# Optimization experiments

Measured on AMD Instinct MI355X. Metric: run time of the kernel, lower is better.

## Reference

```python
import jax, jax.numpy as jnp
import numpy as np

D_K = 128


def setup_inputs() -> dict:
    key = jax.random.key(0)
    k1, k2, k3, k4 = jax.random.split(key, 4)
    return {
        "value_in": jax.random.normal(k1, (4, 2048, 1024), dtype=jnp.float32),
        "w_q": jax.random.normal(k2, (1024, D_K), dtype=jnp.float32),
        "w_k": jax.random.normal(k3, (1024, D_K), dtype=jnp.float32),
        "w_v": jax.random.normal(k4, (1024, 128), dtype=jnp.float32),
    }


def reference(value_in, w_q, w_k, w_v):
    # Projections: [B,S,d_model] @ [d_model,d] -> [B,S,d]
    q = jnp.einsum('bsm,mk->bsk', value_in, w_q)
    k = jnp.einsum('bsm,mk->bsk', value_in, w_k)
    v = jnp.einsum('bsm,mv->bsv', value_in, w_v)
    # Scores [B,S,S], scaled by sqrt(d_k)
    scores = jnp.einsum('bqk,bsk->bqs', q, k) / jnp.sqrt(jnp.float32(D_K))
    S = scores.shape[-1]
    # Causal mask: keep lower triangle (q_idx >= k_idx), -inf elsewhere
    causal = jnp.tril(jnp.ones((S, S), dtype=bool))
    scores = jnp.where(causal, scores, -jnp.inf)
    # NOTE: softmax over the QUERY axis (dim=-2), not the key axis
    attention = jax.nn.softmax(scores, axis=-2)
    out = jnp.einsum('bqs,bsv->bqv', attention, v)
    return out, attention
```

## Files before the change

### kernel.cpp

```cpp
#include <hip/hip_runtime.h>
#include <math.h>

constexpr int B  = 4;
constexpr int S  = 2048;
constexpr int DM = 1024;
constexpr int DK = 128;
constexpr int BS = B * S;
constexpr int NSP = 8;
constexpr int QT  = 16;

static constexpr float SCALE = 0.08838834764831845f;

typedef __attribute__((ext_vector_type(8))) short bf16x8;
typedef __attribute__((ext_vector_type(4))) float f32x4;
typedef __attribute__((ext_vector_type(8))) unsigned short u16x8;

__device__ __forceinline__ unsigned short f2bf(float x) {
  unsigned u = __float_as_uint(x);
  unsigned r = (u + 0x7FFFu + ((u >> 16) & 1u)) >> 16;
  return (unsigned short)r;
}
__device__ __forceinline__ float bf2f(unsigned short h) {
  return __uint_as_float(((unsigned)h) << 16);
}

__device__ __forceinline__ void gload16(const void* g, void* l) {
  __builtin_amdgcn_global_load_lds(
      (const __attribute__((address_space(1))) void*)g,
      (__attribute__((address_space(3))) void*)l, 16, 0, 0);
}

__global__ __launch_bounds__(256) void cvt_hilo(
    const float* __restrict__ x, unsigned short* __restrict__ hi,
    unsigned short* __restrict__ lo)
{
  const size_t idx = (size_t)blockIdx.x * 256 + threadIdx.x;
  const float4 v = ((const float4*)x)[idx];
  ushort4 h, l;
  h.x = f2bf(v.x); l.x = f2bf(v.x - bf2f(h.x));
  h.y = f2bf(v.y); l.y = f2bf(v.y - bf2f(h.y));
  h.z = f2bf(v.z); l.z = f2bf(v.z - bf2f(h.z));
  h.w = f2bf(v.w); l.w = f2bf(v.w - bf2f(h.w));
  ((ushort4*)hi)[idx] = h;
  ((ushort4*)lo)[idx] = l;
}

__global__ void cvtw_kernel(const float* __restrict__ wq, const float* __restrict__ wk,
                            const float* __restrict__ wv,
                            unsigned short* __restrict__ Wth, unsigned short* __restrict__ Wtl)
{
  const int n = blockIdx.x;
  const int p = n >> 7, c = n & 127;
  const float* w = (p == 0) ? wq : (p == 1) ? wk : wv;
  for (int k = threadIdx.x; k < DM; k += 256) {
    const float x = w[(size_t)k * DK + c];
    const unsigned short h = f2bf(x);
    Wth[(size_t)n * DM + k] = h;
    Wtl[(size_t)n * DM + k] = f2bf(x - bf2f(h));
  }
}

__global__ __launch_bounds__(256) void proj_mfma(
    const unsigned short* __restrict__ Ah, const unsigned short* __restrict__ Al,
    const unsigned short* __restrict__ Wh, const unsigned short* __restrict__ Wl,
    unsigned short* __restrict__ qh, unsigned short* __restrict__ ql,
    unsigned short* __restrict__ kh, unsigned short* __restrict__ kl,
    float* __restrict__ vtmp)
{
  __shared__ unsigned short Ash[2][64 * 64];
  __shared__ unsigned short Wsh[2][64 * 64];

  const int r0 = blockIdx.x * 64;
  const int n0 = blockIdx.y * 64;
  const int t  = threadIdx.x;
  const int l  = t & 63, w = t >> 6;
  const int wm = w >> 1, wn = w & 1;
  const int fr = l & 15, kg = l >> 4;

  f32x4 acc[2][2] = {};

  for (int k0 = 0; k0 < DM; k0 += 64) {
    #pragma unroll
    for (int i = 0; i < 2; ++i) {
      const int flat = t + i * 256;
      const int row = flat >> 3, sg = flat & 7;
      const int sgs = sg ^ (row & 7);
      const size_t ga = (size_t)(r0 + row) * DM + k0 + sgs * 8;
      const size_t gw = (size_t)(n0 + row) * DM + k0 + sgs * 8;
      gload16(Ah + ga, &Ash[0][flat * 8]);
      gload16(Al + ga, &Ash[1][flat * 8]);
      gload16(Wh + gw, &Wsh[0][flat * 8]);
      gload16(Wl + gw, &Wsh[1][flat * 8]);
    }
    __syncthreads();

    #pragma unroll
    for (int kk = 0; kk < 2; ++kk) {
      bf16x8 ah[2], al[2], bh[2], bl[2];
      #pragma unroll
      for (int im = 0; im < 2; ++im) {
        const int row = wm * 32 + im * 16 + fr;
        const int off = row * 64 + ((kk * 4 + kg) ^ (row & 7)) * 8;
        ah[im] = *(const bf16x8*)&Ash[0][off];
        al[im] = *(const bf16x8*)&Ash[1][off];
      }
      #pragma unroll
      for (int in = 0; in < 2; ++in) {
        const int row = wn * 32 + in * 16 + fr;
        const int off = row * 64 + ((kk * 4 + kg) ^ (row & 7)) * 8;
        bh[in] = *(const bf16x8*)&Wsh[0][off];
        bl[in] = *(const bf16x8*)&Wsh[1][off];
      }
      #pragma unroll
      for (int im = 0; im < 2; ++im)
        #pragma unroll
        for (int in = 0; in < 2; ++in) {
          acc[im][in] = __builtin_amdgcn_mfma_f32_16x16x32_bf16(ah[im], bh[in], acc[im][in], 0, 0, 0);
          acc[im][in] = __builtin_amdgcn_mfma_f32_16x16x32_bf16(ah[im], bl[in], acc[im][in], 0, 0, 0);
          acc[im][in] = __builtin_amdgcn_mfma_f32_16x16x32_bf16(al[im], bh[in], acc[im][in], 0, 0, 0);
        }
    }
    __syncthreads();
  }

  const int crow = kg * 4;
  #pragma unroll
  for (int im = 0; im < 2; ++im)
    #pragma unroll
    for (int in = 0; in < 2; ++in) {
      const int n = n0 + wn * 32 + in * 16 + fr;
      const int p = n >> 7, c = n & 127;
      #pragma unroll
      for (int r = 0; r < 4; ++r) {
        const int m = r0 + wm * 32 + im * 16 + crow + r;
        const float val = acc[im][in][r];
        if (p == 2) {
          vtmp[(size_t)m * DK + c] = val;
        } else {
          const unsigned short h = f2bf(val);
          const unsigned short lo2 = f2bf(val - bf2f(h));
          unsigned short* hd = p ? kh : qh;
          unsigned short* ld = p ? kl : ql;
          hd[(size_t)m * DK + c] = h;
          ld[(size_t)m * DK + c] = lo2;
        }
      }
    }
}

__global__ __launch_bounds__(256) void cvtv_kernel(
    const float* __restrict__ v, unsigned short* __restrict__ vTh,
    unsigned short* __restrict__ vTl)
{
  const int s0 = blockIdx.x * 64, d0 = blockIdx.y * 64, b = blockIdx.z;
  __shared__ float Ts[64][65];
  const int t = threadIdx.x;
  const int r = t >> 4, c4 = (t & 15) * 4;
  #pragma unroll
  for (int rr = 0; rr < 4; ++rr) {
    const int sl = r + 16 * rr;
    *(float4*)&Ts[sl][c4] =
        *(const float4*)&v[((size_t)b * S + s0 + sl) * DK + d0 + c4];
  }
  __syncthreads();
  const int dl = t >> 2, sq = (t & 3) * 16;
  unsigned short hbuf[16], lbuf[16];
  #pragma unroll
  for (int j = 0; j < 16; ++j) {
    const float val = Ts[sq + j][dl];
    hbuf[j] = f2bf(val);
    lbuf[j] = f2bf(val - bf2f(hbuf[j]));
  }
  const size_t o = (size_t)b * DK * S + (size_t)(d0 + dl) * S + s0 + sq;
  #pragma unroll
  for (int half = 0; half < 2; ++half) {
    *(u16x8*)&vTh[o + half * 8] = *(u16x8*)&hbuf[half * 8];
    *(u16x8*)&vTl[o + half * 8] = *(u16x8*)&lbuf[half * 8];
  }
}

__global__ __launch_bounds__(512) void stats_mfma(
    const unsigned short* __restrict__ qh, const unsigned short* __restrict__ ql,
    const unsigned short* __restrict__ kh, const unsigned short* __restrict__ kl,
    float* __restrict__ pm, float* __restrict__ ps)
{
  const int sp = blockIdx.x, qt = blockIdx.y, b = blockIdx.z;
  const int stmax = 2 * qt + 1;
  if (sp > stmax) return;
  const int q0 = qt * 128;

  __shared__ unsigned short Bsh[2][64 * 128], Bsl[2][64 * 128];
  __shared__ float SmL[64 * 4], SeL[64 * 4];

  const int t = threadIdx.x;
  const int l = t & 63, w = t >> 6;
  const int wm = w >> 1, wn = w & 1;
  const int fr = l & 15, kg = l >> 4;

  #pragma unroll
  for (int i = 0; i < 2; ++i) {
    const int flat = t + i * 512;
    const int row = flat >> 4, sg = flat & 15;
    const int sgs = sg ^ (row & 7);
    const size_t g1 = (size_t)(b * S + q0 + row) * DK + sgs * 8;
    const size_t g2 = (size_t)(b * S + q0 + 64 + row) * DK + sgs * 8;
    gload16(qh + g1, &Bsh[0][flat * 8]);
    gload16(ql + g1, &Bsl[0][flat * 8]);
    gload16(qh + g2, &Bsh[1][flat * 8]);
    gload16(ql + g2, &Bsl[1][flat * 8]);
  }
  __syncthreads();
  bf16x8 qfh[2][4], qfl[2][4];
  {
    const int qbuf = (wm < 2) ? 0 : 1;
    #pragma unroll
    for (int im = 0; im < 2; ++im)
      #pragma unroll
      for (int ks = 0; ks < 4; ++ks) {
        const int qloc = wm * 32 + im * 16 + fr;
        const int row = qloc & 63;
        const int off = row * 128 + ((ks * 4 + kg) ^ (row & 7)) * 8;
        qfh[im][ks] = *(const bf16x8*)&Bsh[qbuf][off];
        qfl[im][ks] = *(const bf16x8*)&Bsl[qbuf][off];
      }
  }
  __syncthreads();

  for (int st = sp; st <= stmax; st += NSP) {
    const int s0 = st * 64;

    #pragma unroll
    for (int i = 0; i < 2; ++i) {
      const int flat = t + i * 512;
      const int row = flat >> 4, sg = flat & 15;
      const int sgs = sg ^ (row & 7);
      const size_t gk = (size_t)(b * S + s0 + row) * DK + sgs * 8;
      gload16(kh + gk, &Bsh[0][flat * 8]);
      gload16(kl + gk, &Bsl[0][flat * 8]);
    }
    __syncthreads();

    f32x4 sacc[2][2] = {};
    #pragma unroll
    for (int ks = 0; ks < 4; ++ks) {
      bf16x8 bh[2], bl[2];
      #pragma unroll
      for (int in = 0; in < 2; ++in) {
        const int row = wn * 32 + in * 16 + fr;
        const int off = row * 128 + ((ks * 4 + kg) ^ (row & 7)) * 8;
        bh[in] = *(const bf16x8*)&Bsh[0][off];
        bl[in] = *(const bf16x8*)&Bsl[0][off];
      }
      #pragma unroll
      for (int im = 0; im < 2; ++im)
        #pragma unroll
        for (int in = 0; in < 2; ++in) {
          sacc[im][in] = __builtin_amdgcn_mfma_f32_16x16x32_bf16(qfh[im][ks], bh[in], sacc[im][in], 0, 0, 0);
          sacc[im][in] = __builtin_amdgcn_mfma_f32_16x16x32_bf16(qfh[im][ks], bl[in], sacc[im][in], 0, 0, 0);
          sacc[im][in] = __builtin_amdgcn_mfma_f32_16x16x32_bf16(qfl[im][ks], bh[in], sacc[im][in], 0, 0, 0);
        }
    }

    const bool mm = (st >= 2 * qt);
    float Sm_[2], Se_[2];
    #pragma unroll
    for (int in = 0; in < 2; ++in) {
      const int scol = s0 + wn * 32 + in * 16 + fr;
      float m8 = -INFINITY;
      #pragma unroll
      for (int im = 0; im < 2; ++im)
        #pragma unroll
        for (int r = 0; r < 4; ++r) {
          const int q = q0 + wm * 32 + im * 16 + kg * 4 + r;
          if (!mm || q >= scol) m8 = fmaxf(m8, sacc[im][in][r] * SCALE);
        }
      float e8 = 0.f;
      if (m8 > -INFINITY) {
        #pragma unroll
        for (int im = 0; im < 2; ++im)
          #pragma unroll
          for (int r = 0; r < 4; ++r) {
            const int q = q0 + wm * 32 + im * 16 + kg * 4 + r;
            if (!mm || q >= scol) e8 += __expf(sacc[im][in][r] * SCALE - m8);
          }
      }
      #pragma unroll
      for (int off = 16; off <= 32; off <<= 1) {
        const float om = __shfl_xor(m8, off);
        const float oe = __shfl_xor(e8, off);
        const float nm = fmaxf(m8, om);
        float ne = 0.f;
        if (m8 > -INFINITY) ne += e8 * __expf(m8 - nm);
        if (om > -INFINITY) ne += oe * __expf(om - nm);
        m8 = nm; e8 = ne;
      }
      Sm_[in] = m8; Se_[in] = e8;
    }
    if (l < 16) {
      #pragma unroll
      for (int in = 0; in < 2; ++in) {
        const int col = wn * 32 + in * 16 + l;
        SmL[col * 4 + wm] = Sm_[in];
        SeL[col * 4 + wm] = Se_[in];
      }
    }
    __syncthreads();
    if (t < 64) {
      float m = -INFINITY;
      #pragma unroll
      for (int y = 0; y < 4; ++y) m = fmaxf(m, SmL[t * 4 + y]);
      float sum = 0.f;
      #pragma unroll
      for (int y = 0; y < 4; ++y) {
        const float my = SmL[t * 4 + y];
        if (my > -INFINITY) sum += SeL[t * 4 + y] * __expf(my - m);
      }
      const size_t o = ((size_t)(b * QT + qt)) * S + s0 + t;
      pm[o] = m;
      ps[o] = sum;
    }
  }
}

__global__ void colcombine_kernel(const float* __restrict__ pm, const float* __restrict__ ps,
                                  float* __restrict__ cm, float* __restrict__ cinv)
{
  const int s = blockIdx.x * 256 + threadIdx.x;
  const int b = blockIdx.y;
  const int ch0 = s >> 7;
  float m = -INFINITY;
  for (int ch = ch0; ch < QT; ++ch)
    m = fmaxf(m, pm[((size_t)(b * QT + ch)) * S + s]);
  float sum = 0.f;
  for (int ch = ch0; ch < QT; ++ch) {
    const size_t i = ((size_t)(b * QT + ch)) * S + s;
    sum += ps[i] * __expf(pm[i] - m);
  }
  cm[(size_t)b * S + s]   = m;
  cinv[(size_t)b * S + s] = 1.f / sum;
}

__global__ void zero_out_kernel(float* __restrict__ out)
{
  const size_t idx = (size_t)blockIdx.x * 256 + threadIdx.x;
  ((float4*)out)[idx] = float4{0.f, 0.f, 0.f, 0.f};
}

__global__ __launch_bounds__(512) void fused_pv(
    const unsigned short* __restrict__ qh, const unsigned short* __restrict__ ql,
    const unsigned short* __restrict__ kh, const unsigned short* __restrict__ kl,
    const unsigned short* __restrict__ vTh, const unsigned short* __restrict__ vTl,
    const float* __restrict__ cm, const float* __restrict__ cinv,
    float* __restrict__ att, float* __restrict__ out)
{
  const int sp = blockIdx.x, qt = blockIdx.y, b = blockIdx.z;
  const int stmax = 2 * qt + 1;
  if (sp > stmax) return;
  const int q0 = qt * 128;
  float* attb = att + (size_t)b * S * S;
  const unsigned short* vth = vTh + (size_t)b * DK * S;
  const unsigned short* vtl = vTl + (size_t)b * DK * S;

  __shared__ unsigned short Ksh[64 * 128], Ksl[64 * 128];
  __shared__ unsigned short Vsh[128 * 64], Vsl[128 * 64];
  __shared__ unsigned short Psh[128 * 64];

  const int t = threadIdx.x;
  const int l = t & 63, w = t >> 6;
  const int wm = w >> 1, wn = w & 1;
  const int fr = l & 15, kg = l >> 4;

  #pragma unroll
  for (int i = 0; i < 2; ++i) {
    const int flat = t + i * 512;
    const int row = flat >> 4, sg = flat & 15;
    const int sgs = sg ^ (row & 7);
    const size_t g1 = (size_t)(b * S + q0 + row) * DK + sgs * 8;
    const size_t g2 = (size_t)(b * S + q0 + 64 + row) * DK + sgs * 8;
    gload16(qh + g1, &Ksh[flat * 8]);
    gload16(ql + g1, &Ksl[flat * 8]);
    gload16(qh + g2, &Vsh[flat * 8]);
    gload16(ql + g2, &Vsl[flat * 8]);
  }
  __syncthreads();
  bf16x8 qfh[2][4], qfl[2][4];
  {
    const unsigned short* qsrc_h = (wm < 2) ? Ksh : Vsh;
    const unsigned short* qsrc_l = (wm < 2) ? Ksl : Vsl;
    #pragma unroll
    for (int im = 0; im < 2; ++im)
      #pragma unroll
      for (int ks = 0; ks < 4; ++ks) {
        const int qloc = wm * 32 + im * 16 + fr;
        const int row = qloc & 63;
        const int off = row * 128 + ((ks * 4 + kg) ^ (row & 7)) * 8;
        qfh[im][ks] = *(const bf16x8*)&qsrc_h[off];
        qfl[im][ks] = *(const bf16x8*)&qsrc_l[off];
      }
  }
  __syncthreads();

  f32x4 acc[8] = {};

  for (int st = sp; st <= stmax; st += NSP) {
    const int s0 = st * 64;

    #pragma unroll
    for (int i = 0; i < 2; ++i) {
      const int flat = t + i * 512;
      const int row = flat >> 4, sg = flat & 15;
      const int sgs = sg ^ (row & 7);
      const size_t gk = (size_t)(b * S + s0 + row) * DK + sgs * 8;
      gload16(kh + gk, &Ksh[flat * 8]);
      gload16(kl + gk, &Ksl[flat * 8]);
    }
    #pragma unroll
    for (int i = 0; i < 2; ++i) {
      const int flat = t + i * 512;
      const int row = flat >> 3, sg = flat & 7;
      const int sgs = sg ^ (row & 7);
      const size_t gv = (size_t)row * S + s0 + sgs * 8;
      gload16(vth + gv, &Vsh[flat * 8]);
      gload16(vtl + gv, &Vsl[flat * 8]);
    }
    __syncthreads();

    f32x4 sacc[2][2] = {};
    #pragma unroll
    for (int ks = 0; ks < 4; ++ks) {
      bf16x8 bh[2], bl[2];
      #pragma unroll
      for (int in = 0; in < 2; ++in) {
        const int row = wn * 32 + in * 16 + fr;
        const int off = row * 128 + ((ks * 4 + kg) ^ (row & 7)) * 8;
        bh[in] = *(const bf16x8*)&Ksh[off];
        bl[in] = *(const bf16x8*)&Ksl[off];
      }
      #pragma unroll
      for (int im = 0; im < 2; ++im)
        #pragma unroll
        for (int in = 0; in < 2; ++in) {
          sacc[im][in] = __builtin_amdgcn_mfma_f32_16x16x32_bf16(qfh[im][ks], bh[in], sacc[im][in], 0, 0, 0);
          sacc[im][in] = __builtin_amdgcn_mfma_f32_16x16x32_bf16(qfh[im][ks], bl[in], sacc[im][in], 0, 0, 0);
          sacc[im][in] = __builtin_amdgcn_mfma_f32_16x16x32_bf16(qfl[im][ks], bh[in], sacc[im][in], 0, 0, 0);
        }
    }

    const bool mm = (st >= 2 * qt);
    #pragma unroll
    for (int in = 0; in < 2; ++in) {
      const int sloc = wn * 32 + in * 16 + fr;
      const int scol = s0 + sloc;
      const float m   = cm[(size_t)b * S + scol];
      const float inv = cinv[(size_t)b * S + scol];
      #pragma unroll
      for (int im = 0; im < 2; ++im) {
        #pragma unroll
        for (int r = 0; r < 4; ++r) {
          const int qloc = wm * 32 + im * 16 + kg * 4 + r;
          const bool live = !mm || (q0 + qloc >= scol);
          const float x = live ? __expf(sacc[im][in][r] * SCALE - m) * inv : 0.f;
          const int idx = qloc * 64 + (((sloc >> 3) ^ (qloc & 7)) * 8 + (sloc & 7));
          Psh[idx] = f2bf(x);
          __builtin_nontemporal_store(x, &attb[(size_t)(q0 + qloc) * S + scol]);
        }
      }
    }

    if (st < 2 * qt) {
      const f32x4 z = {0.f, 0.f, 0.f, 0.f};
      #pragma unroll
      for (int i = 0; i < 4; ++i) {
        const int flat = t + i * 512;
        const int row = flat >> 5, c4 = (flat & 31) * 4;
        __builtin_nontemporal_store(z, (f32x4*)&attb[(size_t)(s0 + row) * S + q0 + c4]);
      }
    }
    __syncthreads();

    #pragma unroll
    for (int ks2 = 0; ks2 < 2; ++ks2) {
      const int arow = w * 16 + fr;
      const int aoff = arow * 64 + ((ks2 * 4 + kg) ^ (arow & 7)) * 8;
      const bf16x8 a = *(const bf16x8*)&Psh[aoff];
      #pragma unroll
      for (int in = 0; in < 8; ++in) {
        const int brow = in * 16 + fr;
        const int boff = brow * 64 + ((ks2 * 4 + kg) ^ (brow & 7)) * 8;
        const bf16x8 b_h = *(const bf16x8*)&Vsh[boff];
        const bf16x8 b_l = *(const bf16x8*)&Vsl[boff];
        acc[in] = __builtin_amdgcn_mfma_f32_16x16x32_bf16(a, b_h, acc[in], 0, 0, 0);
        acc[in] = __builtin_amdgcn_mfma_f32_16x16x32_bf16(a, b_l, acc[in], 0, 0, 0);
      }
    }
    __syncthreads();
  }

  #pragma unroll
  for (int in = 0; in < 8; ++in) {
    #pragma unroll
    for (int r = 0; r < 4; ++r) {
      const int q = q0 + w * 16 + kg * 4 + r;
      const int d = in * 16 + fr;
      atomicAdd(&out[((size_t)b * S + q) * DK + d], acc[in][r]);
    }
  }
}

extern "C" void kernel_launch(void* const* d_in, const int* in_sizes, int n_in,
                              void* d_out, int out_size, void* d_ws, size_t ws_size,
                              hipStream_t stream)
{
  const float* vin = (const float*)d_in[0];
  const float* wq  = (const float*)d_in[1];
  const float* wk  = (const float*)d_in[2];
  const float* wv  = (const float*)d_in[3];

  float* out = (float*)d_out;
  float* att = out + (size_t)B * S * DK;

  unsigned short* Ah  = (unsigned short*)att;
  unsigned short* Al  = Ah  + (size_t)BS * DM;
  unsigned short* Wth = Al  + (size_t)BS * DM;
  unsigned short* Wtl = Wth + (size_t)384 * DM;

  constexpr size_t NE = (size_t)BS * DK;
  unsigned short* qh  = (unsigned short*)d_ws;
  unsigned short* ql  = qh  + NE;
  unsigned short* kh  = ql  + NE;
  unsigned short* kl  = kh  + NE;
  unsigned short* vTh = kl  + NE;
  unsigned short* vTl = vTh + NE;
  float* vtmp = (float*)(vTl + NE);
  float* pm   = vtmp;
  float* ps   = pm + (size_t)QT * B * S;
  float* cm   = ps + (size_t)QT * B * S;
  float* cinv = cm + (size_t)B * S;

  cvt_hilo         <<<dim3(BS * DM / 1024),  256, 0, stream>>>(vin, Ah, Al);
  cvtw_kernel      <<<dim3(384),             256, 0, stream>>>(wq, wk, wv, Wth, Wtl);
  proj_mfma        <<<dim3(128, 6),          256, 0, stream>>>(Ah, Al, Wth, Wtl,
                                                               qh, ql, kh, kl, vtmp);
  cvtv_kernel      <<<dim3(S / 64, 2, B),    256, 0, stream>>>(vtmp, vTh, vTl);
  zero_out_kernel  <<<dim3(BS * DK / 1024),  256, 0, stream>>>(out);
  stats_mfma       <<<dim3(NSP, QT, B),      512, 0, stream>>>(qh, ql, kh, kl, pm, ps);
  colcombine_kernel<<<dim3(S / 256, B),      256, 0, stream>>>(pm, ps, cm, cinv);
  fused_pv         <<<dim3(NSP, QT, B),      512, 0, stream>>>(qh, ql, kh, kl, vTh, vTl,
                                                               cm, cinv, att, out);
}
```

Before: 116.2 us.

## Balance causal attention blocks with a triangular pair enumeration

Replaces the (split, q-tile, batch) grid, where many blocks exited early and large q-tiles looped up to four key tiles, with a flat list of the 136 valid (q-tile, key-pair) combinations per batch. Each block now decodes its pair with a sqrt-based triangular index and processes exactly two 64-wide key tiles, unrolled. This targets load imbalance and idle launched blocks in both the stats and the fused PV kernels. In exchange, the Q tile is reloaded more often and the output gets more partial accumulations per query tile.

New measurement: 129.7 us. 11.5% more time.

```diff
diff --git a/kernel.cpp b/kernel.cpp
--- a/kernel.cpp
+++ b/kernel.cpp
@@ -6,8 +6,8 @@
 constexpr int DM = 1024;
 constexpr int DK = 128;
 constexpr int BS = B * S;
-constexpr int NSP = 8;
 constexpr int QT  = 16;
+constexpr int NPAIR = 136;
 
 static constexpr float SCALE = 0.08838834764831845f;
 
@@ -28,6 +28,14 @@
   __builtin_amdgcn_global_load_lds(
       (const __attribute__((address_space(1))) void*)g,
       (__attribute__((address_space(3))) void*)l, 16, 0, 0);
+}
+
+__device__ __forceinline__ void pair_decode(int i, int& qt, int& sp) {
+  int q = (int)((sqrtf(8.f * i + 1.f) - 1.f) * 0.5f);
+  while ((q + 1) * (q + 2) / 2 <= i) ++q;
+  while (q * (q + 1) / 2 > i) --q;
+  qt = q;
+  sp = i - q * (q + 1) / 2;
 }
 
 __global__ __launch_bounds__(256) void cvt_hilo(
@@ -184,9 +192,9 @@
     const unsigned short* __restrict__ kh, const unsigned short* __restrict__ kl,
     float* __restrict__ pm, float* __restrict__ ps)
 {
-  const int sp = blockIdx.x, qt = blockIdx.y, b = blockIdx.z;
-  const int stmax = 2 * qt + 1;
-  if (sp > stmax) return;
+  int qt, sp;
+  pair_decode(blockIdx.x, qt, sp);
+  const int b = blockIdx.y;
   const int q0 = qt * 128;
 
   __shared__ unsigned short Bsh[2][64 * 128], Bsl[2][64 * 128];
@@ -226,7 +234,9 @@
   }
   __syncthreads();
 
-  for (int st = sp; st <= stmax; st += NSP) {
+  #pragma unroll
+  for (int ii = 0; ii < 2; ++ii) {
+    const int st = 2 * sp + ii;
     const int s0 = st * 64;
 
     #pragma unroll
@@ -353,9 +363,9 @@
     const float* __restrict__ cm, const float* __restrict__ cinv,
     float* __restrict__ att, float* __restrict__ out)
 {
-  const int sp = blockIdx.x, qt = blockIdx.y, b = blockIdx.z;
-  const int stmax = 2 * qt + 1;
-  if (sp > stmax) return;
+  int qt, sp;
+  pair_decode(blockIdx.x, qt, sp);
+  const int b = blockIdx.y;
   const int q0 = qt * 128;
   float* attb = att + (size_t)b * S * S;
   const unsigned short* vth = vTh + (size_t)b * DK * S;
@@ -402,7 +412,9 @@
 
   f32x4 acc[8] = {};
 
-  for (int st = sp; st <= stmax; st += NSP) {
+  #pragma unroll
+  for (int ii = 0; ii < 2; ++ii) {
+    const int st = 2 * sp + ii;
     const int s0 = st * 64;
 
     #pragma unroll
@@ -543,8 +555,8 @@
                                                                qh, ql, kh, kl, vtmp);
   cvtv_kernel      <<<dim3(S / 64, 2, B),    256, 0, stream>>>(vtmp, vTh, vTl);
   zero_out_kernel  <<<dim3(BS * DK / 1024),  256, 0, stream>>>(out);
-  stats_mfma       <<<dim3(NSP, QT, B),      512, 0, stream>>>(qh, ql, kh, kl, pm, ps);
+  stats_mfma       <<<dim3(NPAIR, B),        512, 0, stream>>>(qh, ql, kh, kl, pm, ps);
   colcombine_kernel<<<dim3(S / 256, B),      256, 0, stream>>>(pm, ps, cm, cinv);
-  fused_pv         <<<dim3(NSP, QT, B),      512, 0, stream>>>(qh, ql, kh, kl, vTh, vTl,
+  fused_pv         <<<dim3(NPAIR, B),        512, 0, stream>>>(qh, ql, kh, kl, vTh, vTl,
                                                                cm, cinv, att, out);
 }
```
